# Performance work log

Hardware: AMD Instinct MI355X
Metric: run time of the kernel (lower is better)

Reference implementation:

```python
import jax, jax.numpy as jnp
import numpy as np
from jax import lax

B, T, D_IN, H = 1024, 256, 6, 128
EPS = 1e-5


def layer_norm(x, g, b):
    mu = jnp.mean(x, axis=-1, keepdims=True)
    var = jnp.mean((x - mu) ** 2, axis=-1, keepdims=True)
    return (x - mu) * lax.rsqrt(var + EPS) * g + b


def lstm_dir(x, Wih, Whh, bih, bhh, reverse):
    # x: [B,T,Din]; Wih: [4H,Din]; Whh: [4H,H]. PyTorch gate order: i,f,g,o.
    xp = jnp.einsum('btd,gd->btg', x, Wih) + bih + bhh  # [B,T,4H]
    h0 = jnp.zeros((x.shape[0], Whh.shape[1]), x.dtype)
    c0 = jnp.zeros_like(h0)

    def step(carry, xt):
        h, c = carry
        gates = xt + h @ Whh.T
        i, f, g, o = jnp.split(gates, 4, axis=-1)
        c = jax.nn.sigmoid(f) * c + jax.nn.sigmoid(i) * jnp.tanh(g)
        h = jax.nn.sigmoid(o) * jnp.tanh(c)
        return (h, c), h

    _, hs = lax.scan(step, (h0, c0), jnp.swapaxes(xp, 0, 1), reverse=reverse)
    return jnp.swapaxes(hs, 0, 1)  # [B,T,H], aligned to input time order


def bilstm_layer(x, Wih, Whh, bih, bhh):
    # direction-stacked params: Wih [2,4H,Din], etc.
    fwd = lstm_dir(x, Wih[0], Whh[0], bih[0], bhh[0], reverse=False)
    bwd = lstm_dir(x, Wih[1], Whh[1], bih[1], bhh[1], reverse=True)
    return jnp.concatenate([fwd, bwd], axis=-1)  # [B,T,2H]


def setup_inputs() -> dict:
    key = jax.random.key(0)
    ks = iter(jax.random.split(key, 32))
    u = lambda shape, s: jax.random.uniform(next(ks), shape, jnp.float32, -s, s)
    s_h = 1.0 / np.sqrt(H)
    inp = {
        'x': jax.random.normal(next(ks), (B, T, D_IN), jnp.float32),
        'ln_g': jnp.ones((D_IN,), jnp.float32),
        'ln_b': jnp.zeros((D_IN,), jnp.float32),
        'Wih0': u((2, 4 * H, D_IN), s_h), 'Whh0': u((2, 4 * H, H), s_h),
        'bih0': u((2, 4 * H), s_h), 'bhh0': u((2, 4 * H), s_h),
        'Wih1': u((2, 4 * H, 2 * H), s_h), 'Whh1': u((2, 4 * H, H), s_h),
        'bih1': u((2, 4 * H), s_h), 'bhh1': u((2, 4 * H), s_h),
        'Wa1': u((H, 2 * H), 1.0 / np.sqrt(2 * H)), 'ba1': jnp.zeros((H,), jnp.float32),
        'Wa2': u((1, H), s_h), 'ba2': jnp.zeros((1,), jnp.float32),
        'Wf1': u((H, 2 * H), 1.0 / np.sqrt(2 * H)), 'bf1': jnp.zeros((H,), jnp.float32),
        'ln2_g': jnp.ones((H,), jnp.float32), 'ln2_b': jnp.zeros((H,), jnp.float32),
        'Wf2': u((5, H), s_h),
        'bf2': jnp.array([0.0, 0.0, -0.7, -0.7, 0.0], jnp.float32),
    }
    return inp


def reference(x, ln_g, ln_b, Wih0, Whh0, bih0, bhh0, Wih1, Whh1, bih1, bhh1,
              Wa1, ba1, Wa2, ba2, Wf1, bf1, ln2_g, ln2_b, Wf2, bf2):
    x = layer_norm(x, ln_g, ln_b)
    h = bilstm_layer(x, Wih0, Whh0, bih0, bhh0)       # [B,T,2H]
    h = bilstm_layer(h, Wih1, Whh1, bih1, bhh1)       # [B,T,2H] (eval: no dropout)
    scores = jnp.tanh(h @ Wa1.T + ba1) @ Wa2.T + ba2  # [B,T,1]
    attn = jax.nn.softmax(scores, axis=1)
    context = jnp.sum(h * attn, axis=1)               # [B,2H]
    z = jax.nn.relu(layer_norm(context @ Wf1.T + bf1, ln2_g, ln2_b))
    return z @ Wf2.T + bf2                            # [B,5]
```

## Files before the change

### kernel.cpp

```cpp
#include <hip/hip_runtime.h>
#include <stdint.h>

#define TT 256
#define NS 8
#define CH 8

typedef __attribute__((ext_vector_type(4))) float f32x4;
typedef __attribute__((ext_vector_type(8))) short s16x8;
typedef __attribute__((ext_vector_type(2))) unsigned int u32x2;

#define DEV static __device__ __forceinline__

__device__ uint16_t g_W1f[2*32*8*64*8];

DEV short f2bf(float f){
  union{float f; uint32_t u;} v; v.f = f;
  uint32_t r = v.u + 0x7fffu + ((v.u>>16)&1u);
  return (short)(r>>16);
}
DEV float bf2f(uint32_t u16){
  union{uint32_t u; float f;} v; v.u = u16<<16; return v.f;
}
DEV uint32_t pk2(float a, float b){
  return (uint32_t)(uint16_t)f2bf(a) | ((uint32_t)(uint16_t)f2bf(b)<<16);
}
DEV float rcpf(float x){ return __builtin_amdgcn_rcpf(x); }
DEV float sigm(float x){ return rcpf(1.f + __expf(-x)); }
DEV float tanh_f(float x){ float e = __expf(2.f*x); return 1.f - 2.f*rcpf(e+1.f); }
DEV f32x4 MFMA(s16x8 a, s16x8 b, f32x4 c){
  return __builtin_amdgcn_mfma_f32_16x16x32_bf16(a, b, c, 0, 0, 0);
}
DEV s16x8 cvt8(const float* p){
  f32x4 a = *(const f32x4*)p;
  f32x4 b = *(const f32x4*)(p+4);
  s16x8 o;
  o[0]=f2bf(a[0]); o[1]=f2bf(a[1]); o[2]=f2bf(a[2]); o[3]=f2bf(a[3]);
  o[4]=f2bf(b[0]); o[5]=f2bf(b[1]); o[6]=f2bf(b[2]); o[7]=f2bf(b[3]);
  return o;
}
DEV void bar_lds(){
  asm volatile("s_waitcnt lgkmcnt(0)" ::: "memory");
  __builtin_amdgcn_s_barrier();
}

DEV void flush_step(const short* hb, uint16_t* __restrict__ hdst, int tp,
                    int dir, int BR, int bg, int tid){
  if (tid < 128){
    int row = tid >> 4, part = tid & 15;
    int tg = dir ? (TT-1-tp) : tp;
    s16x8 v = *(const s16x8*)((const char*)hb + row*256 + (((part ^ row)&15)<<4));
    *(s16x8*)(hdst + ((size_t)tg*BR + bg*NS + row)*256 + dir*128 + part*8) = v;
  }
}

__global__ __launch_bounds__(256) void prep_wih1(const float* __restrict__ Wih1)
{
  int tid = blockIdx.x*256 + threadIdx.x;
  int l = tid & 63, kt = (tid>>6)&7, ntg = (tid>>9)&31, dir = (tid>>14)&1;
  int lm = l&15, lk = l>>4;
  int n = ntg*16 + lm;
  s16x8 o = cvt8(Wih1 + ((size_t)(dir*512 + n))*256 + kt*32 + lk*8);
  *(s16x8*)(&g_W1f[(size_t)tid*8]) = o;
}

__global__ __launch_bounds__(512,2) void lstm0_kernel(
    const float* __restrict__ x, const float* __restrict__ lng,
    const float* __restrict__ lnb,
    const float* __restrict__ Wih0, const float* __restrict__ Whh0,
    const float* __restrict__ bih0, const float* __restrict__ bhh0,
    uint16_t* __restrict__ h0, int nb, int BR, int b_off)
{
  const int dir = blockIdx.x / nb, bg = blockIdx.x % nb;
  const int tid = threadIdx.x, w = tid>>6, l = tid&63;
  const int lm = l&15, lk = l>>4;
  const int gb = b_off + bg*NS;

  __shared__ short hbuf[2][2048];
  __shared__ short xnbf[TT*NS*8];
  __shared__ short bxs[8*4*64*8];

  for (int i=tid; i<4096; i+=512) ((short*)hbuf)[i] = 0;

  #pragma unroll
  for (int it=0; it<4; ++it){
    int pr = it*512 + tid;
    int r = pr >> 8, t = pr & 255;
    const float* px = x + ((size_t)(gb+r)*TT + t)*6;
    float v[6]; float mu=0.f, var=0.f;
    #pragma unroll
    for (int d=0; d<6; ++d){ v[d]=px[d]; mu+=v[d]; }
    mu *= (1.f/6.f);
    #pragma unroll
    for (int d=0; d<6; ++d){ float dd=v[d]-mu; var+=dd*dd; }
    float rs = rsqrtf(var*(1.f/6.f) + 1e-5f);
    s16x8 vv;
    #pragma unroll
    for (int d=0; d<6; ++d) vv[d] = f2bf((v[d]-mu)*rs*lng[d] + lnb[d]);
    vv[6]=0; vv[7]=0;
    *(s16x8*)&xnbf[(t*NS + r)*8] = vv;
  }

  const int c = w*16 + lm;
  s16x8 bw[4][4];
  float biasc[4];
  #pragma unroll
  for (int G=0; G<4; ++G){
    const int n = G*128 + c;
    biasc[G] = bih0[dir*512+n] + bhh0[dir*512+n];
    #pragma unroll
    for (int kt=0; kt<4; ++kt)
      bw[G][kt] = cvt8(Whh0 + ((size_t)(dir*512+n))*128 + kt*32 + lk*8);
    s16x8 tx;
    #pragma unroll
    for (int j=0; j<8; ++j){
      int k = lk*8 + j;
      tx[j] = (k<6) ? f2bf(Wih0[(size_t)(dir*512+n)*6 + k]) : (short)0;
    }
    *(s16x8*)&bxs[((w*4+G)*64 + l)*8] = tx;
  }

  const int r0 = ((l>>4)&1)*4 + ((l<32)?0:2);
  float cst[2] = {0.f, 0.f};
  __syncthreads();

  for (int t=0; t<TT; ++t){
    const int tt = dir ? (TT-1-t) : t;
    const int rd = t & 1;
    s16x8 ah[4];
    #pragma unroll
    for (int kt=0; kt<4; ++kt){
      int off = rd*4096 + lm*256 + ((kt*64 + lk*16) ^ (lm<<4));
      ah[kt] = *(const s16x8*)((const char*)hbuf + off);
    }
    s16x8 ax = {0,0,0,0,0,0,0,0};
    if (l < 8) ax = *(const s16x8*)&xnbf[(tt*NS + l)*8];

    f32x4 acc[4];
    #pragma unroll
    for (int G=0; G<4; ++G){
      f32x4 a = {0.f,0.f,0.f,0.f};
      #pragma unroll
      for (int kt=0; kt<4; ++kt) a = MFMA(ah[kt], bw[G][kt], a);
      s16x8 bx = *(const s16x8*)&bxs[((w*4+G)*64 + l)*8];
      a = MFMA(ax, bx, a);
      acc[G] = a;
    }

    float g0[4], g1[4];
    #pragma unroll
    for (int G=0; G<4; ++G){
      float o2 = __shfl(acc[G][2], l & 31);
      float o3 = __shfl(acc[G][3], l & 31);
      g0[G] = ((l<32) ? acc[G][0] : o2) + biasc[G];
      g1[G] = ((l<32) ? acc[G][1] : o3) + biasc[G];
    }
    float hv[2];
    {
      float cc = sigm(g0[1])*cst[0] + sigm(g0[0])*tanh_f(g0[2]);
      cst[0] = cc; hv[0] = sigm(g0[3])*tanh_f(cc);
      cc = sigm(g1[1])*cst[1] + sigm(g1[0])*tanh_f(g1[2]);
      cst[1] = cc; hv[1] = sigm(g1[3])*tanh_f(cc);
    }

    #pragma unroll
    for (int q=0; q<2; ++q){
      int r = r0 + q;
      *(short*)((char*)hbuf + (rd^1)*4096 + r*256 + ((c*2) ^ (r<<4))) = f2bf(hv[q]);
    }
    if (t > 0)
      flush_step(hbuf[rd], h0, t-1, dir, BR, bg, tid);
    bar_lds();
  }
  flush_step(hbuf[0], h0, TT-1, dir, BR, bg, tid);
}

__global__ __launch_bounds__(512,2) void lstm1_kernel(
    const uint16_t* __restrict__ h0,
    const float* __restrict__ Whh1, const float* __restrict__ bih1,
    const float* __restrict__ bhh1, uint16_t* __restrict__ h1,
    int nb, int BR)
{
  const int dir = blockIdx.x / nb, bg = blockIdx.x % nb;
  const int tid = threadIdx.x, w = tid>>6, l = tid&63;
  const int lm = l&15, lk = l>>4;

  __shared__ short hbuf[2][2048];
  __shared__ short abuf[2][16384];
  __shared__ u32x2 xpbuf[8192];

  for (int i=tid; i<4096; i+=512) ((short*)hbuf)[i] = 0;

  const int c = w*16 + lm;
  s16x8 bw[4][4];
  float biasv[4];
  #pragma unroll
  for (int G=0; G<4; ++G){
    const int n = G*128 + c;
    biasv[G] = bih1[dir*512+n] + bhh1[dir*512+n];
    #pragma unroll
    for (int kt=0; kt<4; ++kt)
      bw[G][kt] = cvt8(Whh1 + ((size_t)(dir*512+n))*128 + kt*32 + lk*8);
  }

  const int r0 = ((l>>4)&1)*4 + ((l<32)?0:2);
  float cst[2] = {0.f,0.f};
  s16x8 vst[4];

  #pragma unroll
  for (int it=0; it<4; ++it){
    int sid = it*512 + tid, row = sid>>5, sl = sid&31, s = row>>3, b = row&7;
    int tg = dir ? (TT-1-s) : s;
    vst[it] = *(const s16x8*)(h0 + ((size_t)tg*BR + bg*NS + b)*256 + sl*8);
  }
  #pragma unroll
  for (int it=0; it<4; ++it){
    int sid = it*512 + tid, row = sid>>5, sl = sid&31;
    *(s16x8*)((char*)abuf + row*512 + ((sl ^ (row&15))<<4)) = vst[it];
  }
  __syncthreads();

  for (int ch=0; ch<TT/CH; ++ch){
    const int cur = ch & 1;
    const char* ab = (const char*)abuf + cur*32768;

    if (ch < TT/CH-1){
      #pragma unroll
      for (int it=0; it<4; ++it){
        int sid = it*512 + tid, row = sid>>5, sl = sid&31, s = row>>3, b = row&7;
        int ts = (ch+1)*CH + s;
        int tg = dir ? (TT-1-ts) : ts;
        vst[it] = *(const s16x8*)(h0 + ((size_t)tg*BR + bg*NS + b)*256 + sl*8);
      }
    }

    #pragma unroll
    for (int G=0; G<4; ++G){
      f32x4 acc[4];
      #pragma unroll
      for (int mt=0; mt<4; ++mt) acc[mt] = (f32x4){biasv[G],biasv[G],biasv[G],biasv[G]};
      #pragma unroll
      for (int kt=0; kt<8; ++kt){
        s16x8 bfr = *(const s16x8*)(&g_W1f[(((size_t)(dir*32 + G*8 + w)*8 + kt)*64 + l)*8]);
        #pragma unroll
        for (int mt=0; mt<4; ++mt){
          int row = mt*16 + lm;
          s16x8 afr = *(const s16x8*)(ab + row*512 + (((kt*4+lk) ^ (row&15))<<4));
          acc[mt] = MFMA(afr, bfr, acc[mt]);
        }
      }
      #pragma unroll
      for (int mt=0; mt<4; ++mt){
        u32x2 pw;
        pw[0] = pk2(acc[mt][0], acc[mt][1]);
        pw[1] = pk2(acc[mt][2], acc[mt][3]);
        xpbuf[((w*4+G)*4+mt)*64 + l] = pw;
      }
    }

    if (ch < TT/CH-1){
      char* ab2 = (char*)abuf + (cur^1)*32768;
      #pragma unroll
      for (int it=0; it<4; ++it){
        int sid = it*512 + tid, row = sid>>5, sl = sid&31;
        *(s16x8*)(ab2 + row*512 + ((sl ^ (row&15))<<4)) = vst[it];
      }
    }
    bar_lds();

    #pragma unroll
    for (int s=0; s<CH; ++s){
      const int gs = ch*CH + s;
      const int rd = gs & 1;
      const int lane2 = ((((s&1)<<1) + lk)<<4) + lm;

      f32x4 acc4[4];
      #pragma unroll
      for (int G=0; G<4; ++G){
        u32x2 pw = xpbuf[((w*4+G)*4 + (s>>1))*64 + lane2];
        acc4[G] = (f32x4){bf2f(pw[0]&0xffffu), bf2f(pw[0]>>16),
                          bf2f(pw[1]&0xffffu), bf2f(pw[1]>>16)};
      }

      s16x8 ah[4];
      #pragma unroll
      for (int kt=0; kt<4; ++kt){
        int off = rd*4096 + lm*256 + ((kt*64 + lk*16) ^ (lm<<4));
        ah[kt] = *(const s16x8*)((const char*)hbuf + off);
      }
      #pragma unroll
      for (int G=0; G<4; ++G){
        #pragma unroll
        for (int kt=0; kt<4; ++kt)
          acc4[G] = MFMA(ah[kt], bw[G][kt], acc4[G]);
      }

      float g0[4], g1[4];
      #pragma unroll
      for (int G=0; G<4; ++G){
        float o2 = __shfl(acc4[G][2], l & 31);
        float o3 = __shfl(acc4[G][3], l & 31);
        g0[G] = (l<32) ? acc4[G][0] : o2;
        g1[G] = (l<32) ? acc4[G][1] : o3;
      }
      float hv[2];
      float cc = sigm(g0[1])*cst[0] + sigm(g0[0])*tanh_f(g0[2]);
      cst[0] = cc; hv[0] = sigm(g0[3])*tanh_f(cc);
      cc = sigm(g1[1])*cst[1] + sigm(g1[0])*tanh_f(g1[2]);
      cst[1] = cc; hv[1] = sigm(g1[3])*tanh_f(cc);

      #pragma unroll
      for (int q=0; q<2; ++q){
        int r = r0 + q;
        *(short*)((char*)hbuf + (rd^1)*4096 + r*256 + ((c*2) ^ (r<<4))) = f2bf(hv[q]);
      }
      if (gs > 0)
        flush_step(hbuf[rd], h1, gs-1, dir, BR, bg, tid);
      bar_lds();
    }
  }
  flush_step(hbuf[0], h1, TT-1, dir, BR, bg, tid);
}

__global__ __launch_bounds__(256,2) void scores_kernel(
    const uint16_t* __restrict__ h1, const float* __restrict__ Wa1,
    const float* __restrict__ ba1, const float* __restrict__ Wa2,
    const float* __restrict__ ba2, float* __restrict__ scores,
    int nbb, int BR)
{
  const int bx = blockIdx.x;
  const int t = bx / nbb, bb = (bx - t*nbb) * 64;
  const int tid = threadIdx.x, w = tid>>6, l = tid&63;
  const int lm = l&15, lk = l>>4;
  __shared__ short abuf[64*256];
  __shared__ float scred[4][64];

  #pragma unroll
  for (int it=0; it<8; ++it){
    int sid = it*256 + tid, row = sid>>5, sl = sid&31;
    s16x8 v = *(const s16x8*)(h1 + ((size_t)t*BR + bb + row)*256 + sl*8);
    *(s16x8*)((char*)abuf + row*512 + ((sl ^ (row&15))<<4)) = v;
  }

  s16x8 bwa[2][8]; float b1v[2], wa2v[2];
  #pragma unroll
  for (int nt=0; nt<2; ++nt){
    int n = w*32 + nt*16 + lm;
    b1v[nt] = ba1[n]; wa2v[nt] = Wa2[n];
    #pragma unroll
    for (int kt=0; kt<8; ++kt)
      bwa[nt][kt] = cvt8(Wa1 + (size_t)n*256 + kt*32 + lk*8);
  }
  __syncthreads();

  #pragma unroll
  for (int mt=0; mt<4; ++mt){
    f32x4 a0 = {b1v[0],b1v[0],b1v[0],b1v[0]};
    f32x4 a1 = {b1v[1],b1v[1],b1v[1],b1v[1]};
    #pragma unroll
    for (int kt=0; kt<8; ++kt){
      int row = mt*16 + lm;
      s16x8 af = *(const s16x8*)((const char*)abuf + row*512 + (((kt*4+lk) ^ (row&15))<<4));
      a0 = MFMA(af, bwa[0][kt], a0);
      a1 = MFMA(af, bwa[1][kt], a1);
    }
    #pragma unroll
    for (int j=0; j<4; ++j){
      float pj = tanh_f(a0[j])*wa2v[0] + tanh_f(a1[j])*wa2v[1];
      #pragma unroll
      for (int m=1; m<16; m<<=1) pj += __shfl_xor(pj, m);
      if (lm == 0) scred[w][mt*16 + lk*4 + j] = pj;
    }
  }
  __syncthreads();
  if (tid < 64){
    float s = scred[0][tid]+scred[1][tid]+scred[2][tid]+scred[3][tid] + ba2[0];
    scores[(size_t)(bb+tid)*TT + t] = s;
  }
}

__global__ __launch_bounds__(256,2) void ctx_kernel(
    const uint16_t* __restrict__ h1, const float* __restrict__ scores,
    float* __restrict__ context, int BR)
{
  const int b = blockIdx.x, tid = threadIdx.x;
  __shared__ float at[TT];
  __shared__ float red[8];
  float sc = scores[(size_t)b*TT + tid];
  float m = sc;
  #pragma unroll
  for (int d=1; d<64; d<<=1) m = fmaxf(m, __shfl_xor(m, d));
  if ((tid&63)==0) red[tid>>6] = m;
  __syncthreads();
  m = fmaxf(fmaxf(red[0],red[1]), fmaxf(red[2],red[3]));
  float e = __expf(sc - m);
  float s = e;
  #pragma unroll
  for (int d=1; d<64; d<<=1) s += __shfl_xor(s, d);
  if ((tid&63)==0) red[4+(tid>>6)] = s;
  __syncthreads();
  s = red[4]+red[5]+red[6]+red[7];
  at[tid] = e * rcpf(s);
  __syncthreads();

  float acc = 0.f;
  const uint16_t* hp = h1 + (size_t)b*256 + tid;
  #pragma unroll 8
  for (int t2=0; t2<TT; ++t2) acc += at[t2] * bf2f(hp[(size_t)t2*BR*256]);
  context[(size_t)b*256 + tid] = acc;
}

__global__ __launch_bounds__(128,2) void head_kernel(
    const float* __restrict__ ctx, const float* __restrict__ Wf1,
    const float* __restrict__ bf1, const float* __restrict__ g2,
    const float* __restrict__ b2, const float* __restrict__ Wf2,
    const float* __restrict__ bf2v, float* __restrict__ out, int b_off)
{
  const int b = blockIdx.x, tid = threadIdx.x;
  __shared__ float cx[256];
  __shared__ float zb[128];
  __shared__ float red[4];
  cx[tid]       = ctx[(size_t)b*256 + tid];
  cx[128+tid]   = ctx[(size_t)b*256 + 128 + tid];
  __syncthreads();
  float y = bf1[tid];
  const float* wr = Wf1 + (size_t)tid*256;
  #pragma unroll 8
  for (int k=0; k<256; ++k) y += cx[k]*wr[k];
  float s = y;
  #pragma unroll
  for (int d=1; d<64; d<<=1) s += __shfl_xor(s, d);
  if ((tid&63)==0) red[tid>>6] = s;
  __syncthreads();
  float mu = (red[0]+red[1])*(1.f/128.f);
  float dv = y - mu;
  float q = dv*dv;
  #pragma unroll
  for (int d=1; d<64; d<<=1) q += __shfl_xor(q, d);
  if ((tid&63)==0) red[2+(tid>>6)] = q;
  __syncthreads();
  float var = (red[2]+red[3])*(1.f/128.f);
  float z = dv*rsqrtf(var + 1e-5f)*g2[tid] + b2[tid];
  z = fmaxf(z, 0.f);
  zb[tid] = z;
  __syncthreads();
  if (tid < 5){
    float o = bf2v[tid];
    const float* wp = Wf2 + (size_t)tid*128;
    for (int k=0; k<128; ++k) o += zb[k]*wp[k];
    out[(size_t)(b_off + b)*5 + tid] = o;
  }
}

extern "C" void kernel_launch(void* const* d_in, const int* in_sizes, int n_in,
                              void* d_out, int out_size, void* d_ws, size_t ws_size,
                              hipStream_t stream)
{
  const float* x    = (const float*)d_in[0];
  const float* ln_g = (const float*)d_in[1];
  const float* ln_b = (const float*)d_in[2];
  const float* Wih0 = (const float*)d_in[3];
  const float* Whh0 = (const float*)d_in[4];
  const float* bih0 = (const float*)d_in[5];
  const float* bhh0 = (const float*)d_in[6];
  const float* Wih1 = (const float*)d_in[7];
  const float* Whh1 = (const float*)d_in[8];
  const float* bih1 = (const float*)d_in[9];
  const float* bhh1 = (const float*)d_in[10];
  const float* Wa1  = (const float*)d_in[11];
  const float* ba1  = (const float*)d_in[12];
  const float* Wa2  = (const float*)d_in[13];
  const float* ba2  = (const float*)d_in[14];
  const float* Wf1  = (const float*)d_in[15];
  const float* bf1  = (const float*)d_in[16];
  const float* ln2g = (const float*)d_in[17];
  const float* ln2b = (const float*)d_in[18];
  const float* Wf2  = (const float*)d_in[19];
  const float* bf2  = (const float*)d_in[20];
  float* out = (float*)d_out;

  char* wsb = (char*)d_ws;
  const size_t HBf = (size_t)TT*1024*256*2;

  prep_wih1<<<128, 256, 0, stream>>>(Wih1);

  if (ws_size >= 2*HBf){
    uint16_t* h0 = (uint16_t*)wsb;
    uint16_t* h1 = (uint16_t*)(wsb + HBf);
    float* scoresP = (float*)wsb;
    float* ctxP    = (float*)(wsb + (size_t)1024*TT*4);

    lstm0_kernel<<<256, 512, 0, stream>>>(x, ln_g, ln_b, Wih0, Whh0, bih0, bhh0,
                                          h0, 128, 1024, 0);
    lstm1_kernel<<<256, 512, 0, stream>>>(h0, Whh1, bih1, bhh1, h1, 128, 1024);
    scores_kernel<<<TT*16, 256, 0, stream>>>(h1, Wa1, ba1, Wa2, ba2, scoresP, 16, 1024);
    ctx_kernel   <<<1024, 256, 0, stream>>>(h1, scoresP, ctxP, 1024);
    head_kernel  <<<1024, 128, 0, stream>>>(ctxP, Wf1, bf1, ln2g, ln2b, Wf2, bf2, out, 0);
  } else {
    int BR = 512;
    while (BR > 64){
      size_t HB = (size_t)TT*BR*256*2;
      if (2*HB + 2*((size_t)BR*256*4) <= ws_size) break;
      BR >>= 1;
    }
    const size_t HB = (size_t)TT*BR*256*2;
    uint16_t* h0 = (uint16_t*)wsb;
    uint16_t* h1 = (uint16_t*)(wsb + HB);
    float* scoresP = (float*)(wsb + 2*HB);
    float* ctxP    = (float*)(wsb + 2*HB + (size_t)BR*256*4);
    const int nb = BR/NS;

    for (int b_off = 0; b_off < 1024; b_off += BR){
      lstm0_kernel<<<2*nb, 512, 0, stream>>>(x, ln_g, ln_b, Wih0, Whh0, bih0, bhh0,
                                             h0, nb, BR, b_off);
      lstm1_kernel<<<2*nb, 512, 0, stream>>>(h0, Whh1, bih1, bhh1, h1, nb, BR);
      scores_kernel<<<TT*(BR/64), 256, 0, stream>>>(h1, Wa1, ba1, Wa2, ba2, scoresP,
                                                    BR/64, BR);
      ctx_kernel   <<<BR, 256, 0, stream>>>(h1, scoresP, ctxP, BR);
      head_kernel  <<<BR, 128, 0, stream>>>(ctxP, Wf1, bf1, ln2g, ln2b, Wf2, bf2,
                                            out, b_off);
    }
  }
}
```

Measured before the change: 755.7 us.

## Halve batch rows per LSTM block to double grid size and simplify gate gather

Each LSTM workgroup now handles 4 batch rows instead of 8, so twice as many blocks are launched (512 instead of 256) to fill more compute units on the serial recurrence. The gate-extraction step now uses a shuffle-based select so each lane owns one cell state, and the per-thread work drops accordingly. In lstm1 the double-buffered input-projection staging is replaced by a single buffer with an extra barrier, which shrinks LDS use but adds synchronisation. The cost is that half of each 16-row MFMA tile now holds no useful batch rows.

```diff
diff --git a/kernel.cpp b/kernel.cpp
--- a/kernel.cpp
+++ b/kernel.cpp
@@ -2,7 +2,7 @@
 #include <stdint.h>
 
 #define TT 256
-#define NS 8
+#define NS 4
 #define CH 8
 
 typedef __attribute__((ext_vector_type(4))) float f32x4;
@@ -45,12 +45,22 @@
 
 DEV void flush_step(const short* hb, uint16_t* __restrict__ hdst, int tp,
                     int dir, int BR, int bg, int tid){
-  if (tid < 128){
+  if (tid < 64){
     int row = tid >> 4, part = tid & 15;
     int tg = dir ? (TT-1-tp) : tp;
     s16x8 v = *(const s16x8*)((const char*)hb + row*256 + (((part ^ row)&15)<<4));
     *(s16x8*)(hdst + ((size_t)tg*BR + bg*NS + row)*256 + dir*128 + part*8) = v;
   }
+}
+
+DEV float gsel(const f32x4& a, int lm, int lk){
+  float t0 = __shfl(a[0], lm);
+  float t1 = __shfl(a[1], lm);
+  float t2 = __shfl(a[2], lm);
+  float t3 = __shfl(a[3], lm);
+  float lo = (lk & 1) ? t1 : t0;
+  float hi = (lk & 1) ? t3 : t2;
+  return (lk & 2) ? hi : lo;
 }
 
 __global__ __launch_bounds__(256) void prep_wih1(const float* __restrict__ Wih1)
@@ -82,7 +92,7 @@
   for (int i=tid; i<4096; i+=512) ((short*)hbuf)[i] = 0;
 
   #pragma unroll
-  for (int it=0; it<4; ++it){
+  for (int it=0; it<2; ++it){
     int pr = it*512 + tid;
     int r = pr >> 8, t = pr & 255;
     const float* px = x + ((size_t)(gb+r)*TT + t)*6;
@@ -119,8 +129,7 @@
     *(s16x8*)&bxs[((w*4+G)*64 + l)*8] = tx;
   }
 
-  const int r0 = ((l>>4)&1)*4 + ((l<32)?0:2);
-  float cst[2] = {0.f, 0.f};
+  float cst = 0.f;
   __syncthreads();
 
   for (int t=0; t<TT; ++t){
@@ -133,7 +142,7 @@
       ah[kt] = *(const s16x8*)((const char*)hbuf + off);
     }
     s16x8 ax = {0,0,0,0,0,0,0,0};
-    if (l < 8) ax = *(const s16x8*)&xnbf[(tt*NS + l)*8];
+    if (l < NS) ax = *(const s16x8*)&xnbf[(tt*NS + l)*8];
 
     f32x4 acc[4];
     #pragma unroll
@@ -146,27 +155,15 @@
       acc[G] = a;
     }
 
-    float g0[4], g1[4];
-    #pragma unroll
-    for (int G=0; G<4; ++G){
-      float o2 = __shfl(acc[G][2], l & 31);
-      float o3 = __shfl(acc[G][3], l & 31);
-      g0[G] = ((l<32) ? acc[G][0] : o2) + biasc[G];
-      g1[G] = ((l<32) ? acc[G][1] : o3) + biasc[G];
-    }
-    float hv[2];
-    {
-      float cc = sigm(g0[1])*cst[0] + sigm(g0[0])*tanh_f(g0[2]);
-      cst[0] = cc; hv[0] = sigm(g0[3])*tanh_f(cc);
-      cc = sigm(g1[1])*cst[1] + sigm(g1[0])*tanh_f(g1[2]);
-      cst[1] = cc; hv[1] = sigm(g1[3])*tanh_f(cc);
-    }
-
-    #pragma unroll
-    for (int q=0; q<2; ++q){
-      int r = r0 + q;
-      *(short*)((char*)hbuf + (rd^1)*4096 + r*256 + ((c*2) ^ (r<<4))) = f2bf(hv[q]);
-    }
+    float g0 = gsel(acc[0], lm, lk) + biasc[0];
+    float g1 = gsel(acc[1], lm, lk) + biasc[1];
+    float g2 = gsel(acc[2], lm, lk) + biasc[2];
+    float g3 = gsel(acc[3], lm, lk) + biasc[3];
+    float cc = sigm(g1)*cst + sigm(g0)*tanh_f(g2);
+    cst = cc;
+    float hv = sigm(g3)*tanh_f(cc);
+
+    *(short*)((char*)hbuf + (rd^1)*4096 + lk*256 + ((c*2) ^ (lk<<4))) = f2bf(hv);
     if (t > 0)
       flush_step(hbuf[rd], h0, t-1, dir, BR, bg, tid);
     bar_lds();
@@ -185,8 +182,8 @@
   const int lm = l&15, lk = l>>4;
 
   __shared__ short hbuf[2][2048];
-  __shared__ short abuf[2][16384];
-  __shared__ u32x2 xpbuf[8192];
+  __shared__ short abuf[32*256];
+  __shared__ u32x2 xpbuf[4096];
 
   for (int i=tid; i<4096; i+=512) ((short*)hbuf)[i] = 0;
 
@@ -202,31 +199,27 @@
       bw[G][kt] = cvt8(Whh1 + ((size_t)(dir*512+n))*128 + kt*32 + lk*8);
   }
 
-  const int r0 = ((l>>4)&1)*4 + ((l<32)?0:2);
-  float cst[2] = {0.f,0.f};
-  s16x8 vst[4];
-
-  #pragma unroll
-  for (int it=0; it<4; ++it){
-    int sid = it*512 + tid, row = sid>>5, sl = sid&31, s = row>>3, b = row&7;
+  float cst = 0.f;
+  s16x8 vst[2];
+
+  #pragma unroll
+  for (int it=0; it<2; ++it){
+    int sid = it*512 + tid, row = sid>>5, sl = sid&31, s = row>>2, b = row&3;
     int tg = dir ? (TT-1-s) : s;
     vst[it] = *(const s16x8*)(h0 + ((size_t)tg*BR + bg*NS + b)*256 + sl*8);
   }
   #pragma unroll
-  for (int it=0; it<4; ++it){
+  for (int it=0; it<2; ++it){
     int sid = it*512 + tid, row = sid>>5, sl = sid&31;
     *(s16x8*)((char*)abuf + row*512 + ((sl ^ (row&15))<<4)) = vst[it];
   }
   __syncthreads();
 
   for (int ch=0; ch<TT/CH; ++ch){
-    const int cur = ch & 1;
-    const char* ab = (const char*)abuf + cur*32768;
-
     if (ch < TT/CH-1){
       #pragma unroll
-      for (int it=0; it<4; ++it){
-        int sid = it*512 + tid, row = sid>>5, sl = sid&31, s = row>>3, b = row&7;
+      for (int it=0; it<2; ++it){
+        int sid = it*512 + tid, row = sid>>5, sl = sid&31, s = row>>2, b = row&3;
         int ts = (ch+1)*CH + s;
         int tg = dir ? (TT-1-ts) : ts;
         vst[it] = *(const s16x8*)(h0 + ((size_t)tg*BR + bg*NS + b)*256 + sl*8);
@@ -235,48 +228,47 @@
 
     #pragma unroll
     for (int G=0; G<4; ++G){
-      f32x4 acc[4];
-      #pragma unroll
-      for (int mt=0; mt<4; ++mt) acc[mt] = (f32x4){biasv[G],biasv[G],biasv[G],biasv[G]};
+      f32x4 acc[2];
+      #pragma unroll
+      for (int mt=0; mt<2; ++mt) acc[mt] = (f32x4){biasv[G],biasv[G],biasv[G],biasv[G]};
       #pragma unroll
       for (int kt=0; kt<8; ++kt){
         s16x8 bfr = *(const s16x8*)(&g_W1f[(((size_t)(dir*32 + G*8 + w)*8 + kt)*64 + l)*8]);
         #pragma unroll
-        for (int mt=0; mt<4; ++mt){
+        for (int mt=0; mt<2; ++mt){
           int row = mt*16 + lm;
-          s16x8 afr = *(const s16x8*)(ab + row*512 + (((kt*4+lk) ^ (row&15))<<4));
+          s16x8 afr = *(const s16x8*)((const char*)abuf + row*512 + (((kt*4+lk) ^ (row&15))<<4));
           acc[mt] = MFMA(afr, bfr, acc[mt]);
         }
       }
       #pragma unroll
-      for (int mt=0; mt<4; ++mt){
+      for (int mt=0; mt<2; ++mt){
         u32x2 pw;
         pw[0] = pk2(acc[mt][0], acc[mt][1]);
         pw[1] = pk2(acc[mt][2], acc[mt][3]);
-        xpbuf[((w*4+G)*4+mt)*64 + l] = pw;
-      }
-    }
+        xpbuf[((w*4+G)*2+mt)*64 + l] = pw;
+      }
+    }
+    bar_lds();
 
     if (ch < TT/CH-1){
-      char* ab2 = (char*)abuf + (cur^1)*32768;
-      #pragma unroll
-      for (int it=0; it<4; ++it){
+      #pragma unroll
+      for (int it=0; it<2; ++it){
         int sid = it*512 + tid, row = sid>>5, sl = sid&31;
-        *(s16x8*)(ab2 + row*512 + ((sl ^ (row&15))<<4)) = vst[it];
-      }
-    }
-    bar_lds();
+        *(s16x8*)((char*)abuf + row*512 + ((sl ^ (row&15))<<4)) = vst[it];
+      }
+    }
 
     #pragma unroll
     for (int s=0; s<CH; ++s){
       const int gs = ch*CH + s;
       const int rd = gs & 1;
-      const int lane2 = ((((s&1)<<1) + lk)<<4) + lm;
+      const int lane2 = ((s&3)<<4) + lm;
 
       f32x4 acc4[4];
       #pragma unroll
       for (int G=0; G<4; ++G){
-        u32x2 pw = xpbuf[((w*4+G)*4 + (s>>1))*64 + lane2];
+        u32x2 pw = xpbuf[((w*4+G)*2 + (s>>2))*64 + lane2];
         acc4[G] = (f32x4){bf2f(pw[0]&0xffffu), bf2f(pw[0]>>16),
                           bf2f(pw[1]&0xffffu), bf2f(pw[1]>>16)};
       }
@@ -294,25 +286,15 @@
           acc4[G] = MFMA(ah[kt], bw[G][kt], acc4[G]);
       }
 
-      float g0[4], g1[4];
-      #pragma unroll
-      for (int G=0; G<4; ++G){
-        float o2 = __shfl(acc4[G][2], l & 31);
-        float o3 = __shfl(acc4[G][3], l & 31);
-        g0[G] = (l<32) ? acc4[G][0] : o2;
-        g1[G] = (l<32) ? acc4[G][1] : o3;
-      }
-      float hv[2];
-      float cc = sigm(g0[1])*cst[0] + sigm(g0[0])*tanh_f(g0[2]);
-      cst[0] = cc; hv[0] = sigm(g0[3])*tanh_f(cc);
-      cc = sigm(g1[1])*cst[1] + sigm(g1[0])*tanh_f(g1[2]);
-      cst[1] = cc; hv[1] = sigm(g1[3])*tanh_f(cc);
-
-      #pragma unroll
-      for (int q=0; q<2; ++q){
-        int r = r0 + q;
-        *(short*)((char*)hbuf + (rd^1)*4096 + r*256 + ((c*2) ^ (r<<4))) = f2bf(hv[q]);
-      }
+      float g0 = gsel(acc4[0], lm, lk);
+      float g1 = gsel(acc4[1], lm, lk);
+      float g2 = gsel(acc4[2], lm, lk);
+      float g3 = gsel(acc4[3], lm, lk);
+      float cc = sigm(g1)*cst + sigm(g0)*tanh_f(g2);
+      cst = cc;
+      float hv = sigm(g3)*tanh_f(cc);
+
+      *(short*)((char*)hbuf + (rd^1)*4096 + lk*256 + ((c*2) ^ (lk<<4))) = f2bf(hv);
       if (gs > 0)
         flush_step(hbuf[rd], h1, gs-1, dir, BR, bg, tid);
       bar_lds();
@@ -489,9 +471,9 @@
     float* scoresP = (float*)wsb;
     float* ctxP    = (float*)(wsb + (size_t)1024*TT*4);
 
-    lstm0_kernel<<<256, 512, 0, stream>>>(x, ln_g, ln_b, Wih0, Whh0, bih0, bhh0,
-                                          h0, 128, 1024, 0);
-    lstm1_kernel<<<256, 512, 0, stream>>>(h0, Whh1, bih1, bhh1, h1, 128, 1024);
+    lstm0_kernel<<<512, 512, 0, stream>>>(x, ln_g, ln_b, Wih0, Whh0, bih0, bhh0,
+                                          h0, 256, 1024, 0);
+    lstm1_kernel<<<512, 512, 0, stream>>>(h0, Whh1, bih1, bhh1, h1, 256, 1024);
     scores_kernel<<<TT*16, 256, 0, stream>>>(h1, Wa1, ba1, Wa2, ba2, scoresP, 16, 1024);
     ctx_kernel   <<<1024, 256, 0, stream>>>(h1, scoresP, ctxP, 1024);
     head_kernel  <<<1024, 128, 0, stream>>>(ctxP, Wf1, bf1, ln2g, ln2b, Wf2, bf2, out, 0);
```

New measurement: 1.212 ms. 1.6x slower.

## Add register-resident software-pipelined layer-1 LSTM kernel with runtime spill check

Applied to the files above, without the earlier changes.

Adds a new layer-1 LSTM kernel that computes the input projection for the next 8-step chunk inside the current chunk's recurrent steps. The projection is spread across steps and kept packed as bf16 in registers, which removes the LDS xpbuf staging buffer and interleaves the extra MFMAs with the serial recurrence. It drops the two-blocks-per-SM launch bound to give the kernel more registers. At runtime the host picks this kernel only if it reports no scratch spills, otherwise it falls back to the old kernel. The cost is heavier register use, lower occupancy, and an attribute query on the host every call.

```diff
diff --git a/kernel.cpp b/kernel.cpp
--- a/kernel.cpp
+++ b/kernel.cpp
@@ -174,7 +174,7 @@
   flush_step(hbuf[0], h0, TT-1, dir, BR, bg, tid);
 }
 
-__global__ __launch_bounds__(512,2) void lstm1_kernel(
+__global__ __launch_bounds__(512,2) void lstm1_safe(
     const uint16_t* __restrict__ h0,
     const float* __restrict__ Whh1, const float* __restrict__ bih1,
     const float* __restrict__ bhh1, uint16_t* __restrict__ h1,
@@ -316,6 +316,200 @@
       if (gs > 0)
         flush_step(hbuf[rd], h1, gs-1, dir, BR, bg, tid);
       bar_lds();
+    }
+  }
+  flush_step(hbuf[0], h1, TT-1, dir, BR, bg, tid);
+}
+
+__global__ __launch_bounds__(512) void lstm1_agg(
+    const uint16_t* __restrict__ h0,
+    const float* __restrict__ Whh1, const float* __restrict__ bih1,
+    const float* __restrict__ bhh1, uint16_t* __restrict__ h1,
+    int nb, int BR)
+{
+  const int dir = blockIdx.x / nb, bg = blockIdx.x % nb;
+  const int tid = threadIdx.x, w = tid>>6, l = tid&63;
+  const int lm = l&15, lk = l>>4;
+
+  __shared__ short hbuf[2][2048];
+  __shared__ short abuf[2][16384];
+
+  for (int i=tid; i<4096; i+=512) ((short*)hbuf)[i] = 0;
+
+  const int col = w*16 + lm;
+  s16x8 bw[4][4];
+  float biasv[4];
+  #pragma unroll
+  for (int G=0; G<4; ++G){
+    const int n = G*128 + col;
+    biasv[G] = bih1[dir*512+n] + bhh1[dir*512+n];
+    #pragma unroll
+    for (int kt=0; kt<4; ++kt)
+      bw[G][kt] = cvt8(Whh1 + ((size_t)(dir*512+n))*128 + kt*32 + lk*8);
+  }
+
+  const int r0 = ((l>>4)&1)*4 + ((l<32)?0:2);
+  float cst[2] = {0.f,0.f};
+  uint32_t xpc[4][4][2], xpn[4][4][2];
+  s16x8 vst[4];
+  f32x4 accA[4];
+
+  #pragma unroll
+  for (int it=0; it<4; ++it){
+    int sid = it*512 + tid, row = sid>>5, sl = sid&31, s = row>>3, b = row&7;
+    int tg = dir ? (TT-1-s) : s;
+    vst[it] = *(const s16x8*)(h0 + ((size_t)tg*BR + bg*NS + b)*256 + sl*8);
+  }
+  #pragma unroll
+  for (int it=0; it<4; ++it){
+    int sid = it*512 + tid, row = sid>>5, sl = sid&31;
+    *(s16x8*)((char*)abuf + row*512 + ((sl ^ (row&15))<<4)) = vst[it];
+  }
+  __syncthreads();
+
+  #pragma unroll
+  for (int G=0; G<4; ++G){
+    f32x4 acc[4];
+    #pragma unroll
+    for (int mt=0; mt<4; ++mt) acc[mt] = (f32x4){biasv[G],biasv[G],biasv[G],biasv[G]};
+    #pragma unroll
+    for (int kt=0; kt<8; ++kt){
+      s16x8 bfr = *(const s16x8*)(&g_W1f[(((size_t)(dir*32 + G*8 + w)*8 + kt)*64 + l)*8]);
+      #pragma unroll
+      for (int mt=0; mt<4; ++mt){
+        int row = mt*16 + lm;
+        s16x8 afr = *(const s16x8*)((const char*)abuf + row*512 + (((kt*4+lk) ^ (row&15))<<4));
+        acc[mt] = MFMA(afr, bfr, acc[mt]);
+      }
+    }
+    #pragma unroll
+    for (int mt=0; mt<4; ++mt){
+      xpc[G][mt][0] = pk2(acc[mt][0], acc[mt][1]);
+      xpc[G][mt][1] = pk2(acc[mt][2], acc[mt][3]);
+    }
+  }
+
+  #pragma unroll
+  for (int it=0; it<4; ++it){
+    int sid = it*512 + tid, row = sid>>5, sl = sid&31, s = row>>3, b = row&7;
+    int tg = dir ? (TT-1-(CH+s)) : (CH+s);
+    vst[it] = *(const s16x8*)(h0 + ((size_t)tg*BR + bg*NS + b)*256 + sl*8);
+  }
+  #pragma unroll
+  for (int it=0; it<4; ++it){
+    int sid = it*512 + tid, row = sid>>5, sl = sid&31;
+    *(s16x8*)((char*)abuf + 32768 + row*512 + ((sl ^ (row&15))<<4)) = vst[it];
+  }
+  __syncthreads();
+
+  for (int ck=0; ck<TT/CH; ++ck){
+    const char* abn = (const char*)abuf + ((ck+1)&1)*32768;
+    char* abw = (char*)abuf + (ck&1)*32768;
+
+    if (ck < TT/CH-2){
+      #pragma unroll
+      for (int it=0; it<4; ++it){
+        int sid = it*512 + tid, row = sid>>5, sl = sid&31, s = row>>3, b = row&7;
+        int ts = (ck+2)*CH + s;
+        int tg = dir ? (TT-1-ts) : ts;
+        vst[it] = *(const s16x8*)(h0 + ((size_t)tg*BR + bg*NS + b)*256 + sl*8);
+      }
+    }
+
+    #pragma unroll
+    for (int s=0; s<CH; ++s){
+      const int gs = ck*CH + s;
+      const int rd = gs & 1;
+      const int src = ((((s&1)<<1) + lk)*16 + lm) & 63;
+
+      f32x4 acc4[4];
+      #pragma unroll
+      for (int G=0; G<4; ++G){
+        uint32_t p0 = (uint32_t)__shfl((int)xpc[G][s>>1][0], src);
+        uint32_t p1 = (uint32_t)__shfl((int)xpc[G][s>>1][1], src);
+        acc4[G] = (f32x4){bf2f(p0&0xffffu), bf2f(p0>>16), bf2f(p1&0xffffu), bf2f(p1>>16)};
+      }
+
+      s16x8 ah[4];
+      #pragma unroll
+      for (int kt=0; kt<4; ++kt){
+        int off = rd*4096 + lm*256 + ((kt*64 + lk*16) ^ (lm<<4));
+        ah[kt] = *(const s16x8*)((const char*)hbuf + off);
+      }
+      #pragma unroll
+      for (int G=0; G<4; ++G){
+        #pragma unroll
+        for (int kt=0; kt<4; ++kt)
+          acc4[G] = MFMA(ah[kt], bw[G][kt], acc4[G]);
+      }
+
+      if (ck < TT/CH-1){
+        const int G2 = s>>1;
+        if ((s&1) == 0){
+          #pragma unroll
+          for (int mt=0; mt<4; ++mt) accA[mt] = (f32x4){biasv[G2],biasv[G2],biasv[G2],biasv[G2]};
+        }
+        #pragma unroll
+        for (int kq=0; kq<4; ++kq){
+          const int kt = (s&1)*4 + kq;
+          s16x8 bfr = *(const s16x8*)(&g_W1f[(((size_t)(dir*32 + G2*8 + w)*8 + kt)*64 + l)*8]);
+          #pragma unroll
+          for (int mt=0; mt<4; ++mt){
+            int row = mt*16 + lm;
+            s16x8 afr = *(const s16x8*)(abn + row*512 + (((kt*4+lk) ^ (row&15))<<4));
+            accA[mt] = MFMA(afr, bfr, accA[mt]);
+          }
+        }
+        if (s & 1){
+          #pragma unroll
+          for (int mt=0; mt<4; ++mt){
+            xpn[G2][mt][0] = pk2(accA[mt][0], accA[mt][1]);
+            xpn[G2][mt][1] = pk2(accA[mt][2], accA[mt][3]);
+          }
+        }
+      }
+
+      float g0[4], g1[4];
+      #pragma unroll
+      for (int G=0; G<4; ++G){
+        float o2 = __shfl(acc4[G][2], l & 31);
+        float o3 = __shfl(acc4[G][3], l & 31);
+        g0[G] = (l<32) ? acc4[G][0] : o2;
+        g1[G] = (l<32) ? acc4[G][1] : o3;
+      }
+      float hv[2];
+      float cc = sigm(g0[1])*cst[0] + sigm(g0[0])*tanh_f(g0[2]);
+      cst[0] = cc; hv[0] = sigm(g0[3])*tanh_f(cc);
+      cc = sigm(g1[1])*cst[1] + sigm(g1[0])*tanh_f(g1[2]);
+      cst[1] = cc; hv[1] = sigm(g1[3])*tanh_f(cc);
+
+      #pragma unroll
+      for (int q=0; q<2; ++q){
+        int r = r0 + q;
+        *(short*)((char*)hbuf + (rd^1)*4096 + r*256 + ((col*2) ^ (r<<4))) = f2bf(hv[q]);
+      }
+
+      if (s == 7 && ck < TT/CH-2){
+        #pragma unroll
+        for (int it=0; it<4; ++it){
+          int sid = it*512 + tid, row = sid>>5, sl = sid&31;
+          *(s16x8*)(abw + row*512 + ((sl ^ (row&15))<<4)) = vst[it];
+        }
+      }
+
+      if (gs > 0)
+        flush_step(hbuf[rd], h1, gs-1, dir, BR, bg, tid);
+      bar_lds();
+    }
+
+    if (ck < TT/CH-1){
+      #pragma unroll
+      for (int G=0; G<4; ++G)
+        #pragma unroll
+        for (int mt=0; mt<4; ++mt){
+          xpc[G][mt][0] = xpn[G][mt][0];
+          xpc[G][mt][1] = xpn[G][mt][1];
+        }
     }
   }
   flush_step(hbuf[0], h1, TT-1, dir, BR, bg, tid);
@@ -478,6 +672,14 @@
   const float* bf2  = (const float*)d_in[20];
   float* out = (float*)d_out;
 
+  bool useAgg = false;
+  {
+    hipFuncAttributes fa;
+    if (hipFuncGetAttributes(&fa, (const void*)lstm1_agg) == hipSuccess &&
+        fa.localSizeBytes == 0)
+      useAgg = true;
+  }
+
   char* wsb = (char*)d_ws;
   const size_t HBf = (size_t)TT*1024*256*2;
 
@@ -491,7 +693,10 @@
 
     lstm0_kernel<<<256, 512, 0, stream>>>(x, ln_g, ln_b, Wih0, Whh0, bih0, bhh0,
                                           h0, 128, 1024, 0);
-    lstm1_kernel<<<256, 512, 0, stream>>>(h0, Whh1, bih1, bhh1, h1, 128, 1024);
+    if (useAgg)
+      lstm1_agg <<<256, 512, 0, stream>>>(h0, Whh1, bih1, bhh1, h1, 128, 1024);
+    else
+      lstm1_safe<<<256, 512, 0, stream>>>(h0, Whh1, bih1, bhh1, h1, 128, 1024);
     scores_kernel<<<TT*16, 256, 0, stream>>>(h1, Wa1, ba1, Wa2, ba2, scoresP, 16, 1024);
     ctx_kernel   <<<1024, 256, 0, stream>>>(h1, scoresP, ctxP, 1024);
     head_kernel  <<<1024, 128, 0, stream>>>(ctxP, Wf1, bf1, ln2g, ln2b, Wf2, bf2, out, 0);
@@ -512,7 +717,10 @@
     for (int b_off = 0; b_off < 1024; b_off += BR){
       lstm0_kernel<<<2*nb, 512, 0, stream>>>(x, ln_g, ln_b, Wih0, Whh0, bih0, bhh0,
                                              h0, nb, BR, b_off);
-      lstm1_kernel<<<2*nb, 512, 0, stream>>>(h0, Whh1, bih1, bhh1, h1, nb, BR);
+      if (useAgg)
+        lstm1_agg <<<2*nb, 512, 0, stream>>>(h0, Whh1, bih1, bhh1, h1, nb, BR);
+      else
+        lstm1_safe<<<2*nb, 512, 0, stream>>>(h0, Whh1, bih1, bhh1, h1, nb, BR);
       scores_kernel<<<TT*(BR/64), 256, 0, stream>>>(h1, Wa1, ba1, Wa2, ba2, scoresP,
                                                     BR/64, BR);
       ctx_kernel   <<<BR, 256, 0, stream>>>(h1, scoresP, ctxP, BR);
```

After: 755.8 us. About the same (+0.0%).

## Fold log2e into LSTM gate weights and fuse attention, context and head kernels

Applied to the files above, without the earlier changes.

Pre-scales gate weights and biases by log2(e) (2·log2(e) for the cell gate) so sigmoid and tanh use the hardware exp2 directly, removing a multiply from each transcendental on the recurrent critical path. It also merges the scores, softmax-context and MLP-head kernels into one per-batch-element kernel. This drops the intermediate score and context buffers and two launches. Each block now loops over time in 64-step tiles, giving less parallelism per launch for the attention scoring stage.

```diff
diff --git a/kernel.cpp b/kernel.cpp
--- a/kernel.cpp
+++ b/kernel.cpp
@@ -4,6 +4,8 @@
 #define TT 256
 #define NS 8
 #define CH 8
+#define L2E 1.4426950408889634f
+#define L2E2 2.8853900817779268f
 
 typedef __attribute__((ext_vector_type(4))) float f32x4;
 typedef __attribute__((ext_vector_type(8))) short s16x8;
@@ -25,8 +27,10 @@
   return (uint32_t)(uint16_t)f2bf(a) | ((uint32_t)(uint16_t)f2bf(b)<<16);
 }
 DEV float rcpf(float x){ return __builtin_amdgcn_rcpf(x); }
-DEV float sigm(float x){ return rcpf(1.f + __expf(-x)); }
-DEV float tanh_f(float x){ float e = __expf(2.f*x); return 1.f - 2.f*rcpf(e+1.f); }
+DEV float exp2fast(float x){ return __builtin_amdgcn_exp2f(x); }
+DEV float sigm2(float x){ return rcpf(1.f + exp2fast(-x)); }
+DEV float tanh2(float x){ return 1.f - 2.f*rcpf(exp2fast(x) + 1.f); }
+DEV float tanhr(float x){ return 1.f - 2.f*rcpf(exp2fast(L2E2*x) + 1.f); }
 DEV f32x4 MFMA(s16x8 a, s16x8 b, f32x4 c){
   return __builtin_amdgcn_mfma_f32_16x16x32_bf16(a, b, c, 0, 0, 0);
 }
@@ -38,6 +42,14 @@
   o[4]=f2bf(b[0]); o[5]=f2bf(b[1]); o[6]=f2bf(b[2]); o[7]=f2bf(b[3]);
   return o;
 }
+DEV s16x8 cvt8s(const float* p, float s){
+  f32x4 a = *(const f32x4*)p;
+  f32x4 b = *(const f32x4*)(p+4);
+  s16x8 o;
+  o[0]=f2bf(a[0]*s); o[1]=f2bf(a[1]*s); o[2]=f2bf(a[2]*s); o[3]=f2bf(a[3]*s);
+  o[4]=f2bf(b[0]*s); o[5]=f2bf(b[1]*s); o[6]=f2bf(b[2]*s); o[7]=f2bf(b[3]*s);
+  return o;
+}
 DEV void bar_lds(){
   asm volatile("s_waitcnt lgkmcnt(0)" ::: "memory");
   __builtin_amdgcn_s_barrier();
@@ -59,7 +71,8 @@
   int l = tid & 63, kt = (tid>>6)&7, ntg = (tid>>9)&31, dir = (tid>>14)&1;
   int lm = l&15, lk = l>>4;
   int n = ntg*16 + lm;
-  s16x8 o = cvt8(Wih1 + ((size_t)(dir*512 + n))*256 + kt*32 + lk*8);
+  float sc = ((ntg>>3) == 2) ? L2E2 : L2E;
+  s16x8 o = cvt8s(Wih1 + ((size_t)(dir*512 + n))*256 + kt*32 + lk*8, sc);
   *(s16x8*)(&g_W1f[(size_t)tid*8]) = o;
 }
 
@@ -105,16 +118,17 @@
   float biasc[4];
   #pragma unroll
   for (int G=0; G<4; ++G){
+    const float sc = (G==2) ? L2E2 : L2E;
     const int n = G*128 + c;
-    biasc[G] = bih0[dir*512+n] + bhh0[dir*512+n];
+    biasc[G] = (bih0[dir*512+n] + bhh0[dir*512+n])*sc;
     #pragma unroll
     for (int kt=0; kt<4; ++kt)
-      bw[G][kt] = cvt8(Whh0 + ((size_t)(dir*512+n))*128 + kt*32 + lk*8);
+      bw[G][kt] = cvt8s(Whh0 + ((size_t)(dir*512+n))*128 + kt*32 + lk*8, sc);
     s16x8 tx;
     #pragma unroll
     for (int j=0; j<8; ++j){
       int k = lk*8 + j;
-      tx[j] = (k<6) ? f2bf(Wih0[(size_t)(dir*512+n)*6 + k]) : (short)0;
+      tx[j] = (k<6) ? f2bf(Wih0[(size_t)(dir*512+n)*6 + k]*sc) : (short)0;
     }
     *(s16x8*)&bxs[((w*4+G)*64 + l)*8] = tx;
   }
@@ -156,10 +170,10 @@
     }
     float hv[2];
     {
-      float cc = sigm(g0[1])*cst[0] + sigm(g0[0])*tanh_f(g0[2]);
-      cst[0] = cc; hv[0] = sigm(g0[3])*tanh_f(cc);
-      cc = sigm(g1[1])*cst[1] + sigm(g1[0])*tanh_f(g1[2]);
-      cst[1] = cc; hv[1] = sigm(g1[3])*tanh_f(cc);
+      float cc = sigm2(g0[1])*cst[0] + sigm2(g0[0])*tanh2(g0[2]);
+      cst[0] = cc; hv[0] = sigm2(g0[3])*tanhr(cc);
+      cc = sigm2(g1[1])*cst[1] + sigm2(g1[0])*tanh2(g1[2]);
+      cst[1] = cc; hv[1] = sigm2(g1[3])*tanhr(cc);
     }
 
     #pragma unroll
@@ -195,11 +209,12 @@
   float biasv[4];
   #pragma unroll
   for (int G=0; G<4; ++G){
+    const float sc = (G==2) ? L2E2 : L2E;
     const int n = G*128 + c;
-    biasv[G] = bih1[dir*512+n] + bhh1[dir*512+n];
+    biasv[G] = (bih1[dir*512+n] + bhh1[dir*512+n])*sc;
     #pragma unroll
     for (int kt=0; kt<4; ++kt)
-      bw[G][kt] = cvt8(Whh1 + ((size_t)(dir*512+n))*128 + kt*32 + lk*8);
+      bw[G][kt] = cvt8s(Whh1 + ((size_t)(dir*512+n))*128 + kt*32 + lk*8, sc);
   }
 
   const int r0 = ((l>>4)&1)*4 + ((l<32)?0:2);
@@ -303,10 +318,10 @@
         g1[G] = (l<32) ? acc4[G][1] : o3;
       }
       float hv[2];
-      float cc = sigm(g0[1])*cst[0] + sigm(g0[0])*tanh_f(g0[2]);
-      cst[0] = cc; hv[0] = sigm(g0[3])*tanh_f(cc);
-      cc = sigm(g1[1])*cst[1] + sigm(g1[0])*tanh_f(g1[2]);
-      cst[1] = cc; hv[1] = sigm(g1[3])*tanh_f(cc);
+      float cc = sigm2(g0[1])*cst[0] + sigm2(g0[0])*tanh2(g0[2]);
+      cst[0] = cc; hv[0] = sigm2(g0[3])*tanhr(cc);
+      cc = sigm2(g1[1])*cst[1] + sigm2(g1[0])*tanh2(g1[2]);
+      cst[1] = cc; hv[1] = sigm2(g1[3])*tanhr(cc);
 
       #pragma unroll
       for (int q=0; q<2; ++q){
@@ -321,25 +336,25 @@
   flush_step(hbuf[0], h1, TT-1, dir, BR, bg, tid);
 }
 
-__global__ __launch_bounds__(256,2) void scores_kernel(
-    const uint16_t* __restrict__ h1, const float* __restrict__ Wa1,
-    const float* __restrict__ ba1, const float* __restrict__ Wa2,
-    const float* __restrict__ ba2, float* __restrict__ scores,
-    int nbb, int BR)
+__global__ __launch_bounds__(256,2) void att_kernel(
+    const uint16_t* __restrict__ h1,
+    const float* __restrict__ Wa1, const float* __restrict__ ba1,
+    const float* __restrict__ Wa2, const float* __restrict__ ba2,
+    const float* __restrict__ Wf1, const float* __restrict__ bf1,
+    const float* __restrict__ lg, const float* __restrict__ lb,
+    const float* __restrict__ Wf2, const float* __restrict__ bf2v,
+    float* __restrict__ out, int BR, int b_off)
 {
-  const int bx = blockIdx.x;
-  const int t = bx / nbb, bb = (bx - t*nbb) * 64;
+  const int b = blockIdx.x;
   const int tid = threadIdx.x, w = tid>>6, l = tid&63;
   const int lm = l&15, lk = l>>4;
+
   __shared__ short abuf[64*256];
+  __shared__ float sbuf[TT];
   __shared__ float scred[4][64];
-
-  #pragma unroll
-  for (int it=0; it<8; ++it){
-    int sid = it*256 + tid, row = sid>>5, sl = sid&31;
-    s16x8 v = *(const s16x8*)(h1 + ((size_t)t*BR + bb + row)*256 + sl*8);
-    *(s16x8*)((char*)abuf + row*512 + ((sl ^ (row&15))<<4)) = v;
-  }
+  __shared__ float red[8];
+  __shared__ float cbuf[256];
+  __shared__ float zb[128];
 
   s16x8 bwa[2][8]; float b1v[2], wa2v[2];
   #pragma unroll
@@ -350,98 +365,91 @@
     for (int kt=0; kt<8; ++kt)
       bwa[nt][kt] = cvt8(Wa1 + (size_t)n*256 + kt*32 + lk*8);
   }
-  __syncthreads();
-
-  #pragma unroll
-  for (int mt=0; mt<4; ++mt){
-    f32x4 a0 = {b1v[0],b1v[0],b1v[0],b1v[0]};
-    f32x4 a1 = {b1v[1],b1v[1],b1v[1],b1v[1]};
-    #pragma unroll
-    for (int kt=0; kt<8; ++kt){
-      int row = mt*16 + lm;
-      s16x8 af = *(const s16x8*)((const char*)abuf + row*512 + (((kt*4+lk) ^ (row&15))<<4));
-      a0 = MFMA(af, bwa[0][kt], a0);
-      a1 = MFMA(af, bwa[1][kt], a1);
-    }
-    #pragma unroll
-    for (int j=0; j<4; ++j){
-      float pj = tanh_f(a0[j])*wa2v[0] + tanh_f(a1[j])*wa2v[1];
-      #pragma unroll
-      for (int m=1; m<16; m<<=1) pj += __shfl_xor(pj, m);
-      if (lm == 0) scred[w][mt*16 + lk*4 + j] = pj;
-    }
-  }
-  __syncthreads();
-  if (tid < 64){
-    float s = scred[0][tid]+scred[1][tid]+scred[2][tid]+scred[3][tid] + ba2[0];
-    scores[(size_t)(bb+tid)*TT + t] = s;
-  }
-}
-
-__global__ __launch_bounds__(256,2) void ctx_kernel(
-    const uint16_t* __restrict__ h1, const float* __restrict__ scores,
-    float* __restrict__ context, int BR)
-{
-  const int b = blockIdx.x, tid = threadIdx.x;
-  __shared__ float at[TT];
-  __shared__ float red[8];
-  float sc = scores[(size_t)b*TT + tid];
-  float m = sc;
+
+  for (int tb=0; tb<4; ++tb){
+    const int t0 = tb*64;
+    __syncthreads();
+    #pragma unroll
+    for (int it=0; it<8; ++it){
+      int sid = it*256 + tid, row = sid>>5, sl = sid&31;
+      s16x8 v = *(const s16x8*)(h1 + ((size_t)(t0+row)*BR + b)*256 + sl*8);
+      *(s16x8*)((char*)abuf + row*512 + ((sl ^ (row&15))<<4)) = v;
+    }
+    __syncthreads();
+
+    #pragma unroll
+    for (int mt=0; mt<4; ++mt){
+      f32x4 a0 = {b1v[0],b1v[0],b1v[0],b1v[0]};
+      f32x4 a1 = {b1v[1],b1v[1],b1v[1],b1v[1]};
+      #pragma unroll
+      for (int kt=0; kt<8; ++kt){
+        int row = mt*16 + lm;
+        s16x8 af = *(const s16x8*)((const char*)abuf + row*512 + (((kt*4+lk) ^ (row&15))<<4));
+        a0 = MFMA(af, bwa[0][kt], a0);
+        a1 = MFMA(af, bwa[1][kt], a1);
+      }
+      #pragma unroll
+      for (int j=0; j<4; ++j){
+        float pj = tanhr(a0[j])*wa2v[0] + tanhr(a1[j])*wa2v[1];
+        #pragma unroll
+        for (int m2=1; m2<16; m2<<=1) pj += __shfl_xor(pj, m2);
+        if (lm == 0) scred[w][mt*16 + lk*4 + j] = pj;
+      }
+    }
+    __syncthreads();
+    if (tid < 64)
+      sbuf[t0 + tid] = scred[0][tid]+scred[1][tid]+scred[2][tid]+scred[3][tid] + ba2[0];
+  }
+  __syncthreads();
+
+  float scv = sbuf[tid];
+  float m = scv;
   #pragma unroll
   for (int d=1; d<64; d<<=1) m = fmaxf(m, __shfl_xor(m, d));
-  if ((tid&63)==0) red[tid>>6] = m;
+  if (l == 0) red[w] = m;
   __syncthreads();
   m = fmaxf(fmaxf(red[0],red[1]), fmaxf(red[2],red[3]));
-  float e = __expf(sc - m);
-  float s = e;
-  #pragma unroll
-  for (int d=1; d<64; d<<=1) s += __shfl_xor(s, d);
-  if ((tid&63)==0) red[4+(tid>>6)] = s;
-  __syncthreads();
-  s = red[4]+red[5]+red[6]+red[7];
-  at[tid] = e * rcpf(s);
+  float e = exp2fast(L2E*(scv - m));
+  float ssum = e;
+  #pragma unroll
+  for (int d=1; d<64; d<<=1) ssum += __shfl_xor(ssum, d);
+  if (l == 0) red[4+w] = ssum;
+  __syncthreads();
+  ssum = red[4]+red[5]+red[6]+red[7];
+  sbuf[tid] = e * rcpf(ssum);
   __syncthreads();
 
   float acc = 0.f;
   const uint16_t* hp = h1 + (size_t)b*256 + tid;
   #pragma unroll 8
-  for (int t2=0; t2<TT; ++t2) acc += at[t2] * bf2f(hp[(size_t)t2*BR*256]);
-  context[(size_t)b*256 + tid] = acc;
-}
-
-__global__ __launch_bounds__(128,2) void head_kernel(
-    const float* __restrict__ ctx, const float* __restrict__ Wf1,
-    const float* __restrict__ bf1, const float* __restrict__ g2,
-    const float* __restrict__ b2, const float* __restrict__ Wf2,
-    const float* __restrict__ bf2v, float* __restrict__ out, int b_off)
-{
-  const int b = blockIdx.x, tid = threadIdx.x;
-  __shared__ float cx[256];
-  __shared__ float zb[128];
-  __shared__ float red[4];
-  cx[tid]       = ctx[(size_t)b*256 + tid];
-  cx[128+tid]   = ctx[(size_t)b*256 + 128 + tid];
-  __syncthreads();
-  float y = bf1[tid];
-  const float* wr = Wf1 + (size_t)tid*256;
-  #pragma unroll 8
-  for (int k=0; k<256; ++k) y += cx[k]*wr[k];
-  float s = y;
-  #pragma unroll
-  for (int d=1; d<64; d<<=1) s += __shfl_xor(s, d);
-  if ((tid&63)==0) red[tid>>6] = s;
-  __syncthreads();
-  float mu = (red[0]+red[1])*(1.f/128.f);
+  for (int t2=0; t2<TT; ++t2) acc += sbuf[t2] * bf2f(hp[(size_t)t2*BR*256]);
+  cbuf[tid] = acc;
+  __syncthreads();
+
+  float y = 0.f;
+  if (tid < 128){
+    y = bf1[tid];
+    const float* wr = Wf1 + (size_t)tid*256;
+    #pragma unroll 8
+    for (int k=0; k<256; ++k) y += cbuf[k]*wr[k];
+  }
+  float s2 = y;
+  #pragma unroll
+  for (int d=1; d<64; d<<=1) s2 += __shfl_xor(s2, d);
+  if (l == 0) red[w] = s2;
+  __syncthreads();
+  float mu = (red[0]+red[1]+red[2]+red[3])*(1.f/128.f);
   float dv = y - mu;
-  float q = dv*dv;
+  float q = (tid < 128) ? dv*dv : 0.f;
   #pragma unroll
   for (int d=1; d<64; d<<=1) q += __shfl_xor(q, d);
-  if ((tid&63)==0) red[2+(tid>>6)] = q;
-  __syncthreads();
-  float var = (red[2]+red[3])*(1.f/128.f);
-  float z = dv*rsqrtf(var + 1e-5f)*g2[tid] + b2[tid];
-  z = fmaxf(z, 0.f);
-  zb[tid] = z;
+  if (l == 0) red[4+w] = q;
+  __syncthreads();
+  float var = (red[4]+red[5]+red[6]+red[7])*(1.f/128.f);
+  if (tid < 128){
+    float z = dv*rsqrtf(var + 1e-5f)*lg[tid] + lb[tid];
+    zb[tid] = fmaxf(z, 0.f);
+  }
   __syncthreads();
   if (tid < 5){
     float o = bf2v[tid];
@@ -486,38 +494,30 @@
   if (ws_size >= 2*HBf){
     uint16_t* h0 = (uint16_t*)wsb;
     uint16_t* h1 = (uint16_t*)(wsb + HBf);
-    float* scoresP = (float*)wsb;
-    float* ctxP    = (float*)(wsb + (size_t)1024*TT*4);
 
     lstm0_kernel<<<256, 512, 0, stream>>>(x, ln_g, ln_b, Wih0, Whh0, bih0, bhh0,
                                           h0, 128, 1024, 0);
     lstm1_kernel<<<256, 512, 0, stream>>>(h0, Whh1, bih1, bhh1, h1, 128, 1024);
-    scores_kernel<<<TT*16, 256, 0, stream>>>(h1, Wa1, ba1, Wa2, ba2, scoresP, 16, 1024);
-    ctx_kernel   <<<1024, 256, 0, stream>>>(h1, scoresP, ctxP, 1024);
-    head_kernel  <<<1024, 128, 0, stream>>>(ctxP, Wf1, bf1, ln2g, ln2b, Wf2, bf2, out, 0);
+    att_kernel  <<<1024, 256, 0, stream>>>(h1, Wa1, ba1, Wa2, ba2, Wf1, bf1,
+                                           ln2g, ln2b, Wf2, bf2, out, 1024, 0);
   } else {
     int BR = 512;
     while (BR > 64){
       size_t HB = (size_t)TT*BR*256*2;
-      if (2*HB + 2*((size_t)BR*256*4) <= ws_size) break;
+      if (2*HB <= ws_size) break;
       BR >>= 1;
     }
     const size_t HB = (size_t)TT*BR*256*2;
     uint16_t* h0 = (uint16_t*)wsb;
     uint16_t* h1 = (uint16_t*)(wsb + HB);
-    float* scoresP = (float*)(wsb + 2*HB);
-    float* ctxP    = (float*)(wsb + 2*HB + (size_t)BR*256*4);
     const int nb = BR/NS;
 
     for (int b_off = 0; b_off < 1024; b_off += BR){
       lstm0_kernel<<<2*nb, 512, 0, stream>>>(x, ln_g, ln_b, Wih0, Whh0, bih0, bhh0,
                                              h0, nb, BR, b_off);
       lstm1_kernel<<<2*nb, 512, 0, stream>>>(h0, Whh1, bih1, bhh1, h1, nb, BR);
-      scores_kernel<<<TT*(BR/64), 256, 0, stream>>>(h1, Wa1, ba1, Wa2, ba2, scoresP,
-                                                    BR/64, BR);
-      ctx_kernel   <<<BR, 256, 0, stream>>>(h1, scoresP, ctxP, BR);
-      head_kernel  <<<BR, 128, 0, stream>>>(ctxP, Wf1, bf1, ln2g, ln2b, Wf2, bf2,
-                                            out, b_off);
-    }
-  }
-}
+      att_kernel  <<<BR, 256, 0, stream>>>(h1, Wa1, ba1, Wa2, ba2, Wf1, bf1,
+                                           ln2g, ln2b, Wf2, bf2, out, BR, b_off);
+    }
+  }
+}
```

New measurement: 724.1 us. 1.04x faster.
